# Kernel optimization log

Measured on AMD Instinct MI355X. Metric: run time of the kernel, lower is better.

The kernel has to match this reference:

```python
import jax, jax.numpy as jnp
import numpy as np

E = 8        # num experts
K = 2        # top-k
H = 1024     # hidden size
F = 3584     # intermediate (ffn) size
B, S = 1, 2048


def setup_inputs() -> dict:
    key = jax.random.key(0)
    ks = jax.random.split(key, 5)
    scale_h = 1.0 / np.sqrt(H)
    scale_f = 1.0 / np.sqrt(F)
    return {
        "hidden_states": jax.random.normal(ks[0], (B, S, H), jnp.float32),
        "gate_w": jax.random.normal(ks[1], (E, H), jnp.float32) * scale_h,  # Linear [out,in]
        "w1": jax.random.normal(ks[2], (E, F, H), jnp.float32) * scale_h,
        "w3": jax.random.normal(ks[3], (E, F, H), jnp.float32) * scale_h,
        "w2": jax.random.normal(ks[4], (E, H, F), jnp.float32) * scale_f,
    }


def reference(hidden_states, gate_w, w1, w3, w2):
    b, s, h = hidden_states.shape
    x = hidden_states.reshape(-1, h)                       # [T,H]
    T = x.shape[0]
    # Router: softmax over experts, top-k, renormalize
    router_logits = x @ gate_w.T                           # [T,E]
    routing_weights = jax.nn.softmax(router_logits.astype(jnp.float32), axis=-1)
    topk_w, topk_idx = jax.lax.top_k(routing_weights, K)   # [T,K]
    topk_w = topk_w / jnp.sum(topk_w, axis=-1, keepdims=True)
    # Per-token, per-expert combine weight (0 for unselected experts) --
    # matches the original mask-and-sum over all experts.
    tok = jnp.arange(T)
    expert_weights = jnp.zeros((T, E), jnp.float32).at[tok[:, None], topk_idx].add(topk_w)  # [T,E]
    # Dense per-expert SiLU-gated MLP over all tokens (as the reference loop does),
    # vectorized across experts.
    g = jnp.einsum("th,efh->etf", x, w1)                   # [E,T,F]
    u = jnp.einsum("th,efh->etf", x, w3)                   # [E,T,F]
    act = jax.nn.silu(g) * u                               # [E,T,F]
    y = jnp.einsum("etf,ehf->eth", act, w2)                # [E,T,H]
    out = jnp.einsum("eth,te->th", y, expert_weights.astype(y.dtype))  # [T,H]
    return out.reshape(b, s, h)
```

## Files before the change

kernel.cpp:

```cpp
#include <hip/hip_runtime.h>
#include <hip/hip_bf16.h>

#define T_TOK 2048
#define HID   1024
#define FF    3584
#define NE    8
#define TOPK  2
#define GRIDY 24

typedef __bf16 bf16x8 __attribute__((ext_vector_type(8)));
typedef float  f32x4  __attribute__((ext_vector_type(4)));
typedef unsigned short u16x8 __attribute__((ext_vector_type(8)));

#define WS_COUNTS   0u
#define WS_OFFSETS  64u
#define WS_TILECNT  128u
#define WS_TLE      256u
#define WS_TLM      512u
#define WS_TOPKI    4096u
#define WS_TOPKW    20480u
#define WS_SLOTPOS  36864u
#define WS_SLOTROW  53248u
#define WS_ROUTETOK 69632u
#define WS_XG       131072u
#define WS_ACT      (WS_XG + 4096u*1024u*2u)
#define WS_Y        (WS_ACT + 4096u*3584u*2u)
#define Y_STRIDE    (4096u*1024u)

static __device__ __forceinline__ unsigned short f2bf(float f) {
    unsigned int u = __builtin_bit_cast(unsigned int, f);
    u += 0x7FFFu + ((u >> 16) & 1u);
    return (unsigned short)(u >> 16);
}
static __device__ __forceinline__ unsigned int cvtpk(float lo, float hi) {
    unsigned int r;
    asm("v_cvt_pk_bf16_f32 %0, %1, %2" : "=v"(r) : "v"(lo), "v"(hi));
    return r;
}

__global__ __launch_bounds__(256) void k_router(
    const float* __restrict__ x, const float* __restrict__ gw,
    int* __restrict__ counts, int* __restrict__ topki,
    float* __restrict__ topkw, int* __restrict__ slotpos)
{
    int t = blockIdx.x * 4 + (threadIdx.x >> 6);
    int l = threadIdx.x & 63;
    const float* xr = x + (size_t)t * HID;
    float acc[NE];
#pragma unroll
    for (int e = 0; e < NE; ++e) acc[e] = 0.f;
#pragma unroll
    for (int i = 0; i < 4; ++i) {
        int h = l * 4 + i * 256;
        float4 xv = *(const float4*)(xr + h);
#pragma unroll
        for (int e = 0; e < NE; ++e) {
            float4 g = *(const float4*)(gw + e * HID + h);
            acc[e] += xv.x * g.x + xv.y * g.y + xv.z * g.z + xv.w * g.w;
        }
    }
#pragma unroll
    for (int e = 0; e < NE; ++e) {
#pragma unroll
        for (int off = 32; off; off >>= 1) acc[e] += __shfl_xor(acc[e], off);
    }
    if (l == 0) {
        float best = -1e30f, second = -1e30f;
        int bi = 0, si = 0;
#pragma unroll
        for (int e = 0; e < NE; ++e) {
            float v = acc[e];
            if (v > best) { second = best; si = bi; best = v; bi = e; }
            else if (v > second) { second = v; si = e; }
        }
        float w0 = 1.f / (1.f + __expf(second - best));
        float w1 = 1.f - w0;
        topki[2 * t] = bi;  topki[2 * t + 1] = si;
        topkw[2 * t] = w0;  topkw[2 * t + 1] = w1;
        slotpos[2 * t]     = atomicAdd(&counts[bi], 1);
        slotpos[2 * t + 1] = atomicAdd(&counts[si], 1);
    }
}

__global__ void k_prefix(const int* __restrict__ counts, int* __restrict__ offsets,
                         int* __restrict__ tle, int* __restrict__ tlm,
                         int* __restrict__ tilecnt) {
    if (threadIdx.x == 0) {
        int o = 0;
#pragma unroll
        for (int e = 0; e < NE; ++e) { offsets[e] = o; o += counts[e]; }
        int n = 0;
        for (int e = 0; e < NE; ++e) {
            int t = (counts[e] + 255) >> 8;
            for (int i = 0; i < t; ++i) { tle[n] = e; tlm[n] = i; ++n; }
        }
        tilecnt[0] = n;
    }
}

__global__ __launch_bounds__(256) void k_fillgather(
    const float* __restrict__ x, const int* __restrict__ topki,
    const int* __restrict__ slotpos, const int* __restrict__ offsets,
    int* __restrict__ routetok, int* __restrict__ slotrow,
    unsigned short* __restrict__ xg)
{
    int j = blockIdx.x;
    int e = topki[j];
    int row = offsets[e] + slotpos[j];
    int tok = j >> 1;
    if (threadIdx.x == 0) {
        routetok[row] = tok;
        slotrow[j] = row;
    }
    int c = threadIdx.x * 4;
    float4 v = *(const float4*)(x + (size_t)tok * HID + c);
    ushort4 o;
    o.x = f2bf(v.x); o.y = f2bf(v.y); o.z = f2bf(v.z); o.w = f2bf(v.w);
    int sc = c ^ ((row & 7) << 3);
    *(ushort4*)(xg + (size_t)row * HID + sc) = o;
}

__global__ __launch_bounds__(512, 4) void k_gemm1(
    const unsigned short* __restrict__ xg, const float* __restrict__ w1,
    const float* __restrict__ w3, const int* __restrict__ counts,
    const int* __restrict__ offsets, const int* __restrict__ tle,
    const int* __restrict__ tlm, const int* __restrict__ tilecnt,
    unsigned short* __restrict__ act)
{
    int d = blockIdx.x;
    int xcd = d & 7, s = d >> 3;
    int fhi = s % 7, by = s / 7;
    int fx = xcd + 8 * fhi;
    if (by >= tilecnt[0]) return;
    int e = tle[by];
    int rbase = tlm[by] * 256;
    int cnt = counts[e], obase = offsets[e];
    int fbase = fx * 64;

    __shared__ __align__(16) unsigned short lA[256 * 64];
    __shared__ __align__(16) unsigned short lB1[64 * 64];
    __shared__ __align__(16) unsigned short lB3[64 * 64];

    int tid = threadIdx.x;
    const int ra0 = tid >> 3, ca = (tid & 7) * 8;
    const int rb0 = tid >> 4, cb = (tid & 15) * 4;
    const unsigned short* pa[4];
#pragma unroll
    for (int i = 0; i < 4; ++i) {
        int r = obase + rbase + ra0 + 64 * i;
        if (r > 4095) r = 4095;
        pa[i] = xg + (size_t)r * HID + ca;
    }
    const float* w1e = w1 + ((size_t)e * FF + fbase) * HID;
    const float* w3e = w3 + ((size_t)e * FF + fbase) * HID;
    const float* pb1[2];
    const float* pb3[2];
    int wba[2];
#pragma unroll
    for (int i = 0; i < 2; ++i) {
        int row = rb0 + 32 * i;
        pb1[i] = w1e + (size_t)row * HID + cb;
        pb3[i] = w3e + (size_t)row * HID + cb;
        wba[i] = row * 64 + (cb ^ ((row & 7) << 3));
    }

    int lane = tid & 63, wv = tid >> 6, wr = wv >> 1, wc = wv & 1;
    int klane = (lane >> 4) * 8;
    int swzA = (((obase & 7) + (lane & 7)) & 7) << 3;
    int swzB = (lane & 7) << 3;
    f32x4 accg[4][2], accu[4][2];
#pragma unroll
    for (int m = 0; m < 4; ++m)
#pragma unroll
        for (int n = 0; n < 2; ++n) {
            accg[m][n] = (f32x4){0.f, 0.f, 0.f, 0.f};
            accu[m][n] = (f32x4){0.f, 0.f, 0.f, 0.f};
        }

    u16x8 ra[4]; float4 r1[2], r3[2];
#pragma unroll
    for (int i = 0; i < 4; ++i) ra[i] = *(const u16x8*)(pa[i]);
#pragma unroll
    for (int i = 0; i < 2; ++i) { r1[i] = *(const float4*)(pb1[i]); r3[i] = *(const float4*)(pb3[i]); }

    for (int kt = 0; kt < HID / 64; ++kt) {
#pragma unroll
        for (int i = 0; i < 4; ++i)
            *(u16x8*)(lA + (ra0 + 64 * i) * 64 + ca) = ra[i];
#pragma unroll
        for (int i = 0; i < 2; ++i) {
            uint2 p;
            p.x = cvtpk(r1[i].x, r1[i].y); p.y = cvtpk(r1[i].z, r1[i].w);
            *(uint2*)(lB1 + wba[i]) = p;
            p.x = cvtpk(r3[i].x, r3[i].y); p.y = cvtpk(r3[i].z, r3[i].w);
            *(uint2*)(lB3 + wba[i]) = p;
        }
        __syncthreads();
        if (kt < HID / 64 - 1) {
            int kof = (kt + 1) * 64;
#pragma unroll
            for (int i = 0; i < 4; ++i) ra[i] = *(const u16x8*)(pa[i] + kof);
#pragma unroll
            for (int i = 0; i < 2; ++i) {
                r1[i] = *(const float4*)(pb1[i] + kof);
                r3[i] = *(const float4*)(pb3[i] + kof);
            }
        }
#pragma unroll
        for (int kk = 0; kk < 64; kk += 32) {
            int kc = kk + klane;
            int kA = kc ^ swzA, kB = kc ^ swzB;
            bf16x8 a[4], b1[2], b3[2];
#pragma unroll
            for (int m = 0; m < 4; ++m)
                a[m] = *(const bf16x8*)(lA + (wr * 64 + m * 16 + (lane & 15)) * 64 + kA);
#pragma unroll
            for (int n = 0; n < 2; ++n) {
                b1[n] = *(const bf16x8*)(lB1 + (wc * 32 + n * 16 + (lane & 15)) * 64 + kB);
                b3[n] = *(const bf16x8*)(lB3 + (wc * 32 + n * 16 + (lane & 15)) * 64 + kB);
            }
#pragma unroll
            for (int m = 0; m < 4; ++m)
#pragma unroll
                for (int n = 0; n < 2; ++n) {
                    accg[m][n] = __builtin_amdgcn_mfma_f32_16x16x32_bf16(a[m], b1[n], accg[m][n], 0, 0, 0);
                    accu[m][n] = __builtin_amdgcn_mfma_f32_16x16x32_bf16(a[m], b3[n], accu[m][n], 0, 0, 0);
                }
        }
        __syncthreads();
    }

#pragma unroll
    for (int m = 0; m < 4; ++m)
#pragma unroll
        for (int n = 0; n < 2; ++n)
#pragma unroll
            for (int r = 0; r < 4; ++r) {
                int lr = wr * 64 + m * 16 + (lane >> 4) * 4 + r;
                if (rbase + lr < cnt) {
                    float g = accg[m][n][r], u = accu[m][n][r];
                    float s = g / (1.f + __expf(-g));
                    int row = obase + rbase + lr;
                    int col = fbase + wc * 32 + n * 16 + (lane & 15);
                    int scol = col ^ ((row & 7) << 3);
                    act[(size_t)row * FF + scol] = f2bf(s * u);
                }
            }
}

__global__ __launch_bounds__(512, 4) void k_gemm2(
    const unsigned short* __restrict__ act, const float* __restrict__ w2,
    const int* __restrict__ counts, const int* __restrict__ offsets,
    const int* __restrict__ tle, const int* __restrict__ tlm,
    const int* __restrict__ tilecnt, float* __restrict__ y, int ks)
{
    int d = blockIdx.x;
    int hx = d & 7, s = d >> 3;
    int z = s % 3, by = s / 3;
    if (by >= tilecnt[0]) return;
    if (z >= ks) return;
    int e = tle[by];
    int rbase = tlm[by] * 256;
    int cnt = counts[e], obase = offsets[e];
    int hbase = hx * 128;
    const int KTOT = FF / 64;
    int per = (KTOT + ks - 1) / ks;
    int kt0 = z * per;
    int ktn = (KTOT < kt0 + per ? KTOT : kt0 + per) - kt0;
    int kb0 = kt0 * 64;

    __shared__ __align__(16) unsigned short lA[256 * 64];
    __shared__ __align__(16) unsigned short lB[128 * 64];

    int tid = threadIdx.x;
    const int ra0 = tid >> 3, ca = (tid & 7) * 8;
    const unsigned short* pa[4];
#pragma unroll
    for (int i = 0; i < 4; ++i) {
        int r = obase + rbase + ra0 + 64 * i;
        if (r > 4095) r = 4095;
        pa[i] = act + (size_t)r * FF + kb0 + ca;
    }
    int hr = tid >> 2, cbf = (tid & 3) * 16;
    const float* pb = w2 + ((size_t)e * HID + hbase + hr) * FF + kb0 + cbf;
    int wbb[2];
#pragma unroll
    for (int g = 0; g < 2; ++g)
        wbb[g] = hr * 64 + ((cbf + g * 8) ^ ((hr & 7) << 3));

    int lane = tid & 63, wv = tid >> 6;
    int wr = wv & 3, wc = wv >> 2;
    int klane = (lane >> 4) * 8;
    int swzA = (((obase & 7) + (lane & 7)) & 7) << 3;
    int swzB = (lane & 7) << 3;
    f32x4 acc[4][4];
#pragma unroll
    for (int m = 0; m < 4; ++m)
#pragma unroll
        for (int n = 0; n < 4; ++n) acc[m][n] = (f32x4){0.f, 0.f, 0.f, 0.f};

    u16x8 ra[4]; float4 rw[4];
#pragma unroll
    for (int i = 0; i < 4; ++i) ra[i] = *(const u16x8*)(pa[i]);
#pragma unroll
    for (int j = 0; j < 4; ++j) rw[j] = *(const float4*)(pb + 4 * j);

    for (int kt = 0; kt < ktn; ++kt) {
#pragma unroll
        for (int i = 0; i < 4; ++i)
            *(u16x8*)(lA + (ra0 + 64 * i) * 64 + ca) = ra[i];
#pragma unroll
        for (int g = 0; g < 2; ++g) {
            uint4 q;
            q.x = cvtpk(rw[2 * g].x, rw[2 * g].y);
            q.y = cvtpk(rw[2 * g].z, rw[2 * g].w);
            q.z = cvtpk(rw[2 * g + 1].x, rw[2 * g + 1].y);
            q.w = cvtpk(rw[2 * g + 1].z, rw[2 * g + 1].w);
            *(uint4*)(lB + wbb[g]) = q;
        }
        __syncthreads();
        if (kt < ktn - 1) {
            int kof = (kt + 1) * 64;
#pragma unroll
            for (int i = 0; i < 4; ++i) ra[i] = *(const u16x8*)(pa[i] + kof);
#pragma unroll
            for (int j = 0; j < 4; ++j) rw[j] = *(const float4*)(pb + kof + 4 * j);
        }
#pragma unroll
        for (int kk = 0; kk < 64; kk += 32) {
            int kc = kk + klane;
            int kA = kc ^ swzA, kB = kc ^ swzB;
            bf16x8 a[4], b[4];
#pragma unroll
            for (int m = 0; m < 4; ++m)
                a[m] = *(const bf16x8*)(lA + (wr * 64 + m * 16 + (lane & 15)) * 64 + kA);
#pragma unroll
            for (int n = 0; n < 4; ++n)
                b[n] = *(const bf16x8*)(lB + (wc * 64 + n * 16 + (lane & 15)) * 64 + kB);
#pragma unroll
            for (int m = 0; m < 4; ++m)
#pragma unroll
                for (int n = 0; n < 4; ++n)
                    acc[m][n] = __builtin_amdgcn_mfma_f32_16x16x32_bf16(a[m], b[n], acc[m][n], 0, 0, 0);
        }
        __syncthreads();
    }

    float* yz = y + (size_t)z * Y_STRIDE;
#pragma unroll
    for (int m = 0; m < 4; ++m)
#pragma unroll
        for (int n = 0; n < 4; ++n)
#pragma unroll
            for (int r = 0; r < 4; ++r) {
                int lr = wr * 64 + m * 16 + (lane >> 4) * 4 + r;
                if (rbase + lr < cnt) {
                    int col = hbase + wc * 64 + n * 16 + (lane & 15);
                    yz[(size_t)(obase + rbase + lr) * HID + col] = acc[m][n][r];
                }
            }
}

__global__ void k_combine(const float* __restrict__ y, const int* __restrict__ slotrow,
                          const float* __restrict__ topkw, float* __restrict__ out, int ks) {
    int j = blockIdx.x * blockDim.x + threadIdx.x;
    int t = j >> 8, c = j & 255;
    int r0 = slotrow[2 * t], r1 = slotrow[2 * t + 1];
    float w0 = topkw[2 * t], w1 = topkw[2 * t + 1];
    float4 a = {0.f, 0.f, 0.f, 0.f}, b = {0.f, 0.f, 0.f, 0.f};
    for (int z = 0; z < ks; ++z) {
        const float4* yz = (const float4*)(y + (size_t)z * Y_STRIDE);
        float4 av = yz[(size_t)r0 * 256 + c];
        float4 bv = yz[(size_t)r1 * 256 + c];
        a.x += av.x; a.y += av.y; a.z += av.z; a.w += av.w;
        b.x += bv.x; b.y += bv.y; b.z += bv.z; b.w += bv.w;
    }
    float4 o;
    o.x = w0 * a.x + w1 * b.x;
    o.y = w0 * a.y + w1 * b.y;
    o.z = w0 * a.z + w1 * b.z;
    o.w = w0 * a.w + w1 * b.w;
    ((float4*)out)[j] = o;
}

extern "C" void kernel_launch(void* const* d_in, const int* in_sizes, int n_in,
                              void* d_out, int out_size, void* d_ws, size_t ws_size,
                              hipStream_t stream) {
    const float* x  = (const float*)d_in[0];
    const float* gw = (const float*)d_in[1];
    const float* w1 = (const float*)d_in[2];
    const float* w3 = (const float*)d_in[3];
    const float* w2 = (const float*)d_in[4];
    float* out = (float*)d_out;

    char* ws = (char*)d_ws;
    int*   counts   = (int*)(ws + WS_COUNTS);
    int*   offsets  = (int*)(ws + WS_OFFSETS);
    int*   tilecnt  = (int*)(ws + WS_TILECNT);
    int*   tle      = (int*)(ws + WS_TLE);
    int*   tlm      = (int*)(ws + WS_TLM);
    int*   topki    = (int*)(ws + WS_TOPKI);
    float* topkw    = (float*)(ws + WS_TOPKW);
    int*   slotpos  = (int*)(ws + WS_SLOTPOS);
    int*   slotrow  = (int*)(ws + WS_SLOTROW);
    int*   routetok = (int*)(ws + WS_ROUTETOK);
    unsigned short* xg   = (unsigned short*)(ws + WS_XG);
    unsigned short* actb = (unsigned short*)(ws + WS_ACT);
    float* yb = (float*)(ws + WS_Y);

    size_t ybytes = (size_t)Y_STRIDE * 4;
    int ks = (ws_size >= (size_t)WS_Y + 3 * ybytes) ? 3 : 2;

    hipMemsetAsync(counts, 0, 64, stream);
    k_router<<<T_TOK / 4, 256, 0, stream>>>(x, gw, counts, topki, topkw, slotpos);
    k_prefix<<<1, 64, 0, stream>>>(counts, offsets, tle, tlm, tilecnt);
    k_fillgather<<<T_TOK * TOPK, 256, 0, stream>>>(x, topki, slotpos, offsets, routetok, slotrow, xg);
    k_gemm1<<<56 * GRIDY, 512, 0, stream>>>(xg, w1, w3, counts, offsets, tle, tlm, tilecnt, actb);
    k_gemm2<<<8 * 3 * GRIDY, 512, 0, stream>>>(actb, w2, counts, offsets, tle, tlm, tilecnt, yb, ks);
    k_combine<<<2048, 256, 0, stream>>>(yb, slotrow, topkw, out, ks);
}
```

Before: 265.2 us.

## Process pairs of row tiles per gemm1 block and switch to 2D/3D grids

gemm1 blocks now loop over up to two consecutive 256-row tiles of the same expert, reusing one block's weight column slice, with a new paired tile list built in the prefix kernel. Both GEMMs drop the XCD-interleaved 1D block index mapping in favour of plain multi-dimensional grids. The aim is fewer gemm1 blocks and a partial reuse of weight addressing per block. The trade-off is less parallelism and a serialized second tile in each block, with no weight data kept across tiles (it is reloaded from global). Dropping the XCD-aware ordering may also hurt L2 locality.

Result: slower. 306.0 us (+15.4%).

```diff
diff --git a/kernel.cpp b/kernel.cpp
--- a/kernel.cpp
+++ b/kernel.cpp
@@ -6,7 +6,8 @@
 #define FF    3584
 #define NE    8
 #define TOPK  2
-#define GRIDY 24
+#define GRIDY  24
+#define GRIDYP 16
 
 typedef __bf16 bf16x8 __attribute__((ext_vector_type(8)));
 typedef float  f32x4  __attribute__((ext_vector_type(4)));
@@ -17,6 +18,8 @@
 #define WS_TILECNT  128u
 #define WS_TLE      256u
 #define WS_TLM      512u
+#define WS_TLPE     1280u
+#define WS_TLPM     1536u
 #define WS_TOPKI    4096u
 #define WS_TOPKW    20480u
 #define WS_SLOTPOS  36864u
@@ -84,17 +87,19 @@
 
 __global__ void k_prefix(const int* __restrict__ counts, int* __restrict__ offsets,
                          int* __restrict__ tle, int* __restrict__ tlm,
+                         int* __restrict__ tlpe, int* __restrict__ tlpm,
                          int* __restrict__ tilecnt) {
     if (threadIdx.x == 0) {
         int o = 0;
 #pragma unroll
         for (int e = 0; e < NE; ++e) { offsets[e] = o; o += counts[e]; }
-        int n = 0;
+        int n = 0, np = 0;
         for (int e = 0; e < NE; ++e) {
             int t = (counts[e] + 255) >> 8;
             for (int i = 0; i < t; ++i) { tle[n] = e; tlm[n] = i; ++n; }
-        }
-        tilecnt[0] = n;
+            for (int i = 0; i < t; i += 2) { tlpe[np] = e; tlpm[np] = i; ++np; }
+        }
+        tilecnt[0] = n; tilecnt[1] = np;
     }
 }
 
@@ -123,19 +128,17 @@
 __global__ __launch_bounds__(512, 4) void k_gemm1(
     const unsigned short* __restrict__ xg, const float* __restrict__ w1,
     const float* __restrict__ w3, const int* __restrict__ counts,
-    const int* __restrict__ offsets, const int* __restrict__ tle,
-    const int* __restrict__ tlm, const int* __restrict__ tilecnt,
+    const int* __restrict__ offsets, const int* __restrict__ tlpe,
+    const int* __restrict__ tlpm, const int* __restrict__ tilecnt,
     unsigned short* __restrict__ act)
 {
-    int d = blockIdx.x;
-    int xcd = d & 7, s = d >> 3;
-    int fhi = s % 7, by = s / 7;
-    int fx = xcd + 8 * fhi;
-    if (by >= tilecnt[0]) return;
-    int e = tle[by];
-    int rbase = tlm[by] * 256;
+    int bp = blockIdx.y;
+    if (bp >= tilecnt[1]) return;
+    int e = tlpe[bp];
+    int m0 = tlpm[bp];
     int cnt = counts[e], obase = offsets[e];
-    int fbase = fx * 64;
+    int ntile = (cnt + 255) >> 8;
+    int fbase = blockIdx.x * 64;
 
     __shared__ __align__(16) unsigned short lA[256 * 64];
     __shared__ __align__(16) unsigned short lB1[64 * 64];
@@ -144,13 +147,6 @@
     int tid = threadIdx.x;
     const int ra0 = tid >> 3, ca = (tid & 7) * 8;
     const int rb0 = tid >> 4, cb = (tid & 15) * 4;
-    const unsigned short* pa[4];
-#pragma unroll
-    for (int i = 0; i < 4; ++i) {
-        int r = obase + rbase + ra0 + 64 * i;
-        if (r > 4095) r = 4095;
-        pa[i] = xg + (size_t)r * HID + ca;
-    }
     const float* w1e = w1 + ((size_t)e * FF + fbase) * HID;
     const float* w3e = w3 + ((size_t)e * FF + fbase) * HID;
     const float* pb1[2];
@@ -168,84 +164,99 @@
     int klane = (lane >> 4) * 8;
     int swzA = (((obase & 7) + (lane & 7)) & 7) << 3;
     int swzB = (lane & 7) << 3;
-    f32x4 accg[4][2], accu[4][2];
-#pragma unroll
-    for (int m = 0; m < 4; ++m)
-#pragma unroll
-        for (int n = 0; n < 2; ++n) {
-            accg[m][n] = (f32x4){0.f, 0.f, 0.f, 0.f};
-            accu[m][n] = (f32x4){0.f, 0.f, 0.f, 0.f};
-        }
-
-    u16x8 ra[4]; float4 r1[2], r3[2];
-#pragma unroll
-    for (int i = 0; i < 4; ++i) ra[i] = *(const u16x8*)(pa[i]);
-#pragma unroll
-    for (int i = 0; i < 2; ++i) { r1[i] = *(const float4*)(pb1[i]); r3[i] = *(const float4*)(pb3[i]); }
-
-    for (int kt = 0; kt < HID / 64; ++kt) {
-#pragma unroll
-        for (int i = 0; i < 4; ++i)
-            *(u16x8*)(lA + (ra0 + 64 * i) * 64 + ca) = ra[i];
-#pragma unroll
-        for (int i = 0; i < 2; ++i) {
-            uint2 p;
-            p.x = cvtpk(r1[i].x, r1[i].y); p.y = cvtpk(r1[i].z, r1[i].w);
-            *(uint2*)(lB1 + wba[i]) = p;
-            p.x = cvtpk(r3[i].x, r3[i].y); p.y = cvtpk(r3[i].z, r3[i].w);
-            *(uint2*)(lB3 + wba[i]) = p;
-        }
-        __syncthreads();
-        if (kt < HID / 64 - 1) {
-            int kof = (kt + 1) * 64;
-#pragma unroll
-            for (int i = 0; i < 4; ++i) ra[i] = *(const u16x8*)(pa[i] + kof);
+
+    for (int h = 0; h < 2; ++h) {
+        int mt = m0 + h;
+        if (mt >= ntile) break;
+        int rbase = mt * 256;
+
+        const unsigned short* pa[4];
+#pragma unroll
+        for (int i = 0; i < 4; ++i) {
+            int r = obase + rbase + ra0 + 64 * i;
+            if (r > 4095) r = 4095;
+            pa[i] = xg + (size_t)r * HID + ca;
+        }
+
+        f32x4 accg[4][2], accu[4][2];
+#pragma unroll
+        for (int m = 0; m < 4; ++m)
+#pragma unroll
+            for (int n = 0; n < 2; ++n) {
+                accg[m][n] = (f32x4){0.f, 0.f, 0.f, 0.f};
+                accu[m][n] = (f32x4){0.f, 0.f, 0.f, 0.f};
+            }
+
+        u16x8 ra[4]; float4 r1[2], r3[2];
+#pragma unroll
+        for (int i = 0; i < 4; ++i) ra[i] = *(const u16x8*)(pa[i]);
+#pragma unroll
+        for (int i = 0; i < 2; ++i) { r1[i] = *(const float4*)(pb1[i]); r3[i] = *(const float4*)(pb3[i]); }
+
+        for (int kt = 0; kt < HID / 64; ++kt) {
+#pragma unroll
+            for (int i = 0; i < 4; ++i)
+                *(u16x8*)(lA + (ra0 + 64 * i) * 64 + ca) = ra[i];
 #pragma unroll
             for (int i = 0; i < 2; ++i) {
-                r1[i] = *(const float4*)(pb1[i] + kof);
-                r3[i] = *(const float4*)(pb3[i] + kof);
+                uint2 p;
+                p.x = cvtpk(r1[i].x, r1[i].y); p.y = cvtpk(r1[i].z, r1[i].w);
+                *(uint2*)(lB1 + wba[i]) = p;
+                p.x = cvtpk(r3[i].x, r3[i].y); p.y = cvtpk(r3[i].z, r3[i].w);
+                *(uint2*)(lB3 + wba[i]) = p;
             }
-        }
-#pragma unroll
-        for (int kk = 0; kk < 64; kk += 32) {
-            int kc = kk + klane;
-            int kA = kc ^ swzA, kB = kc ^ swzB;
-            bf16x8 a[4], b1[2], b3[2];
-#pragma unroll
-            for (int m = 0; m < 4; ++m)
-                a[m] = *(const bf16x8*)(lA + (wr * 64 + m * 16 + (lane & 15)) * 64 + kA);
-#pragma unroll
-            for (int n = 0; n < 2; ++n) {
-                b1[n] = *(const bf16x8*)(lB1 + (wc * 32 + n * 16 + (lane & 15)) * 64 + kB);
-                b3[n] = *(const bf16x8*)(lB3 + (wc * 32 + n * 16 + (lane & 15)) * 64 + kB);
-            }
-#pragma unroll
-            for (int m = 0; m < 4; ++m)
-#pragma unroll
-                for (int n = 0; n < 2; ++n) {
-                    accg[m][n] = __builtin_amdgcn_mfma_f32_16x16x32_bf16(a[m], b1[n], accg[m][n], 0, 0, 0);
-                    accu[m][n] = __builtin_amdgcn_mfma_f32_16x16x32_bf16(a[m], b3[n], accu[m][n], 0, 0, 0);
-                }
-        }
-        __syncthreads();
-    }
-
-#pragma unroll
-    for (int m = 0; m < 4; ++m)
-#pragma unroll
-        for (int n = 0; n < 2; ++n)
-#pragma unroll
-            for (int r = 0; r < 4; ++r) {
-                int lr = wr * 64 + m * 16 + (lane >> 4) * 4 + r;
-                if (rbase + lr < cnt) {
-                    float g = accg[m][n][r], u = accu[m][n][r];
-                    float s = g / (1.f + __expf(-g));
-                    int row = obase + rbase + lr;
-                    int col = fbase + wc * 32 + n * 16 + (lane & 15);
-                    int scol = col ^ ((row & 7) << 3);
-                    act[(size_t)row * FF + scol] = f2bf(s * u);
+            __syncthreads();
+            if (kt < HID / 64 - 1) {
+                int kof = (kt + 1) * 64;
+#pragma unroll
+                for (int i = 0; i < 4; ++i) ra[i] = *(const u16x8*)(pa[i] + kof);
+#pragma unroll
+                for (int i = 0; i < 2; ++i) {
+                    r1[i] = *(const float4*)(pb1[i] + kof);
+                    r3[i] = *(const float4*)(pb3[i] + kof);
                 }
             }
+#pragma unroll
+            for (int kk = 0; kk < 64; kk += 32) {
+                int kc = kk + klane;
+                int kA = kc ^ swzA, kB = kc ^ swzB;
+                bf16x8 a[4], b1[2], b3[2];
+#pragma unroll
+                for (int m = 0; m < 4; ++m)
+                    a[m] = *(const bf16x8*)(lA + (wr * 64 + m * 16 + (lane & 15)) * 64 + kA);
+#pragma unroll
+                for (int n = 0; n < 2; ++n) {
+                    b1[n] = *(const bf16x8*)(lB1 + (wc * 32 + n * 16 + (lane & 15)) * 64 + kB);
+                    b3[n] = *(const bf16x8*)(lB3 + (wc * 32 + n * 16 + (lane & 15)) * 64 + kB);
+                }
+#pragma unroll
+                for (int m = 0; m < 4; ++m)
+#pragma unroll
+                    for (int n = 0; n < 2; ++n) {
+                        accg[m][n] = __builtin_amdgcn_mfma_f32_16x16x32_bf16(a[m], b1[n], accg[m][n], 0, 0, 0);
+                        accu[m][n] = __builtin_amdgcn_mfma_f32_16x16x32_bf16(a[m], b3[n], accu[m][n], 0, 0, 0);
+                    }
+            }
+            __syncthreads();
+        }
+
+#pragma unroll
+        for (int m = 0; m < 4; ++m)
+#pragma unroll
+            for (int n = 0; n < 2; ++n)
+#pragma unroll
+                for (int r = 0; r < 4; ++r) {
+                    int lr = wr * 64 + m * 16 + (lane >> 4) * 4 + r;
+                    if (rbase + lr < cnt) {
+                        float g = accg[m][n][r], u = accu[m][n][r];
+                        float s = g / (1.f + __expf(-g));
+                        int row = obase + rbase + lr;
+                        int col = fbase + wc * 32 + n * 16 + (lane & 15);
+                        int scol = col ^ ((row & 7) << 3);
+                        act[(size_t)row * FF + scol] = f2bf(s * u);
+                    }
+                }
+    }
 }
 
 __global__ __launch_bounds__(512, 4) void k_gemm2(
@@ -254,15 +265,13 @@
     const int* __restrict__ tle, const int* __restrict__ tlm,
     const int* __restrict__ tilecnt, float* __restrict__ y, int ks)
 {
-    int d = blockIdx.x;
-    int hx = d & 7, s = d >> 3;
-    int z = s % 3, by = s / 3;
+    int by = blockIdx.y;
     if (by >= tilecnt[0]) return;
-    if (z >= ks) return;
     int e = tle[by];
     int rbase = tlm[by] * 256;
     int cnt = counts[e], obase = offsets[e];
-    int hbase = hx * 128;
+    int hbase = blockIdx.x * 128;
+    int z = blockIdx.z;
     const int KTOT = FF / 64;
     int per = (KTOT + ks - 1) / ks;
     int kt0 = z * per;
@@ -399,6 +408,8 @@
     int*   tilecnt  = (int*)(ws + WS_TILECNT);
     int*   tle      = (int*)(ws + WS_TLE);
     int*   tlm      = (int*)(ws + WS_TLM);
+    int*   tlpe     = (int*)(ws + WS_TLPE);
+    int*   tlpm     = (int*)(ws + WS_TLPM);
     int*   topki    = (int*)(ws + WS_TOPKI);
     float* topkw    = (float*)(ws + WS_TOPKW);
     int*   slotpos  = (int*)(ws + WS_SLOTPOS);
@@ -413,9 +424,9 @@
 
     hipMemsetAsync(counts, 0, 64, stream);
     k_router<<<T_TOK / 4, 256, 0, stream>>>(x, gw, counts, topki, topkw, slotpos);
-    k_prefix<<<1, 64, 0, stream>>>(counts, offsets, tle, tlm, tilecnt);
+    k_prefix<<<1, 64, 0, stream>>>(counts, offsets, tle, tlm, tlpe, tlpm, tilecnt);
     k_fillgather<<<T_TOK * TOPK, 256, 0, stream>>>(x, topki, slotpos, offsets, routetok, slotrow, xg);
-    k_gemm1<<<56 * GRIDY, 512, 0, stream>>>(xg, w1, w3, counts, offsets, tle, tlm, tilecnt, actb);
-    k_gemm2<<<8 * 3 * GRIDY, 512, 0, stream>>>(actb, w2, counts, offsets, tle, tlm, tilecnt, yb, ks);
+    k_gemm1<<<dim3(FF / 64, GRIDYP, 1), 512, 0, stream>>>(xg, w1, w3, counts, offsets, tlpe, tlpm, tilecnt, actb);
+    k_gemm2<<<dim3(HID / 128, GRIDY, ks), 512, 0, stream>>>(actb, w2, counts, offsets, tle, tlm, tilecnt, yb, ks);
     k_combine<<<2048, 256, 0, stream>>>(yb, slotrow, topkw, out, ks);
 }
```

## Widen gemm1 N-tile to 128 columns and drop XCD-aware block mapping

Applied to the files above, without the earlier changes.

The gate/up GEMM block tile grows from 256x64 to 256x128 along F, with the warp layout changed to 4x2 and each thread loading 32 contiguous fp32 weights. The goal is to halve how often the gathered activation tile is re-read from memory and to raise MFMA work per LDS sync. The cost is doubled accumulator registers (launch bounds drop from 4 to 2 blocks per SM) and fewer blocks. Both GEMMs also switch from a hand-linearised XCD-aware block index to a plain 2D/3D grid, which removes the explicit per-XCD L2 grouping.

Result: slower. 337.4 us (+27.2%).

```diff
diff --git a/kernel.cpp b/kernel.cpp
--- a/kernel.cpp
+++ b/kernel.cpp
@@ -120,30 +120,26 @@
     *(ushort4*)(xg + (size_t)row * HID + sc) = o;
 }
 
-__global__ __launch_bounds__(512, 4) void k_gemm1(
+__global__ __launch_bounds__(512, 2) void k_gemm1(
     const unsigned short* __restrict__ xg, const float* __restrict__ w1,
     const float* __restrict__ w3, const int* __restrict__ counts,
     const int* __restrict__ offsets, const int* __restrict__ tle,
     const int* __restrict__ tlm, const int* __restrict__ tilecnt,
     unsigned short* __restrict__ act)
 {
-    int d = blockIdx.x;
-    int xcd = d & 7, s = d >> 3;
-    int fhi = s % 7, by = s / 7;
-    int fx = xcd + 8 * fhi;
+    int by = blockIdx.y;
     if (by >= tilecnt[0]) return;
     int e = tle[by];
     int rbase = tlm[by] * 256;
     int cnt = counts[e], obase = offsets[e];
-    int fbase = fx * 64;
+    int fbase = blockIdx.x * 128;
 
     __shared__ __align__(16) unsigned short lA[256 * 64];
-    __shared__ __align__(16) unsigned short lB1[64 * 64];
-    __shared__ __align__(16) unsigned short lB3[64 * 64];
+    __shared__ __align__(16) unsigned short lB1[128 * 64];
+    __shared__ __align__(16) unsigned short lB3[128 * 64];
 
     int tid = threadIdx.x;
     const int ra0 = tid >> 3, ca = (tid & 7) * 8;
-    const int rb0 = tid >> 4, cb = (tid & 15) * 4;
     const unsigned short* pa[4];
 #pragma unroll
     for (int i = 0; i < 4; ++i) {
@@ -151,49 +147,46 @@
         if (r > 4095) r = 4095;
         pa[i] = xg + (size_t)r * HID + ca;
     }
-    const float* w1e = w1 + ((size_t)e * FF + fbase) * HID;
-    const float* w3e = w3 + ((size_t)e * FF + fbase) * HID;
-    const float* pb1[2];
-    const float* pb3[2];
-    int wba[2];
-#pragma unroll
-    for (int i = 0; i < 2; ++i) {
-        int row = rb0 + 32 * i;
-        pb1[i] = w1e + (size_t)row * HID + cb;
-        pb3[i] = w3e + (size_t)row * HID + cb;
-        wba[i] = row * 64 + (cb ^ ((row & 7) << 3));
-    }
-
-    int lane = tid & 63, wv = tid >> 6, wr = wv >> 1, wc = wv & 1;
+    int mb = tid >> 8, rb = (tid >> 1) & 127, kh = tid & 1;
+    const float* pb = (mb ? w3 : w1) + ((size_t)e * FF + fbase + rb) * HID + kh * 32;
+    unsigned short* lB = mb ? lB3 : lB1;
+    int wbb[4];
+#pragma unroll
+    for (int g = 0; g < 4; ++g)
+        wbb[g] = rb * 64 + ((kh * 32 + g * 8) ^ ((rb & 7) << 3));
+
+    int lane = tid & 63, wv = tid >> 6;
+    int wr = wv & 3, wc = wv >> 2;
     int klane = (lane >> 4) * 8;
     int swzA = (((obase & 7) + (lane & 7)) & 7) << 3;
     int swzB = (lane & 7) << 3;
-    f32x4 accg[4][2], accu[4][2];
+    f32x4 accg[4][4], accu[4][4];
 #pragma unroll
     for (int m = 0; m < 4; ++m)
 #pragma unroll
-        for (int n = 0; n < 2; ++n) {
+        for (int n = 0; n < 4; ++n) {
             accg[m][n] = (f32x4){0.f, 0.f, 0.f, 0.f};
             accu[m][n] = (f32x4){0.f, 0.f, 0.f, 0.f};
         }
 
-    u16x8 ra[4]; float4 r1[2], r3[2];
+    u16x8 ra[4]; float4 rw[8];
 #pragma unroll
     for (int i = 0; i < 4; ++i) ra[i] = *(const u16x8*)(pa[i]);
 #pragma unroll
-    for (int i = 0; i < 2; ++i) { r1[i] = *(const float4*)(pb1[i]); r3[i] = *(const float4*)(pb3[i]); }
+    for (int j = 0; j < 8; ++j) rw[j] = *(const float4*)(pb + 4 * j);
 
     for (int kt = 0; kt < HID / 64; ++kt) {
 #pragma unroll
         for (int i = 0; i < 4; ++i)
             *(u16x8*)(lA + (ra0 + 64 * i) * 64 + ca) = ra[i];
 #pragma unroll
-        for (int i = 0; i < 2; ++i) {
-            uint2 p;
-            p.x = cvtpk(r1[i].x, r1[i].y); p.y = cvtpk(r1[i].z, r1[i].w);
-            *(uint2*)(lB1 + wba[i]) = p;
-            p.x = cvtpk(r3[i].x, r3[i].y); p.y = cvtpk(r3[i].z, r3[i].w);
-            *(uint2*)(lB3 + wba[i]) = p;
+        for (int g = 0; g < 4; ++g) {
+            uint4 q;
+            q.x = cvtpk(rw[2 * g].x, rw[2 * g].y);
+            q.y = cvtpk(rw[2 * g].z, rw[2 * g].w);
+            q.z = cvtpk(rw[2 * g + 1].x, rw[2 * g + 1].y);
+            q.w = cvtpk(rw[2 * g + 1].z, rw[2 * g + 1].w);
+            *(uint4*)(lB + wbb[g]) = q;
         }
         __syncthreads();
         if (kt < HID / 64 - 1) {
@@ -201,30 +194,27 @@
 #pragma unroll
             for (int i = 0; i < 4; ++i) ra[i] = *(const u16x8*)(pa[i] + kof);
 #pragma unroll
-            for (int i = 0; i < 2; ++i) {
-                r1[i] = *(const float4*)(pb1[i] + kof);
-                r3[i] = *(const float4*)(pb3[i] + kof);
-            }
+            for (int j = 0; j < 8; ++j) rw[j] = *(const float4*)(pb + kof + 4 * j);
         }
 #pragma unroll
         for (int kk = 0; kk < 64; kk += 32) {
             int kc = kk + klane;
             int kA = kc ^ swzA, kB = kc ^ swzB;
-            bf16x8 a[4], b1[2], b3[2];
+            bf16x8 a[4], b1f[4], b3f[4];
 #pragma unroll
             for (int m = 0; m < 4; ++m)
                 a[m] = *(const bf16x8*)(lA + (wr * 64 + m * 16 + (lane & 15)) * 64 + kA);
 #pragma unroll
-            for (int n = 0; n < 2; ++n) {
-                b1[n] = *(const bf16x8*)(lB1 + (wc * 32 + n * 16 + (lane & 15)) * 64 + kB);
-                b3[n] = *(const bf16x8*)(lB3 + (wc * 32 + n * 16 + (lane & 15)) * 64 + kB);
+            for (int n = 0; n < 4; ++n) {
+                b1f[n] = *(const bf16x8*)(lB1 + (wc * 64 + n * 16 + (lane & 15)) * 64 + kB);
+                b3f[n] = *(const bf16x8*)(lB3 + (wc * 64 + n * 16 + (lane & 15)) * 64 + kB);
             }
 #pragma unroll
             for (int m = 0; m < 4; ++m)
 #pragma unroll
-                for (int n = 0; n < 2; ++n) {
-                    accg[m][n] = __builtin_amdgcn_mfma_f32_16x16x32_bf16(a[m], b1[n], accg[m][n], 0, 0, 0);
-                    accu[m][n] = __builtin_amdgcn_mfma_f32_16x16x32_bf16(a[m], b3[n], accu[m][n], 0, 0, 0);
+                for (int n = 0; n < 4; ++n) {
+                    accg[m][n] = __builtin_amdgcn_mfma_f32_16x16x32_bf16(a[m], b1f[n], accg[m][n], 0, 0, 0);
+                    accu[m][n] = __builtin_amdgcn_mfma_f32_16x16x32_bf16(a[m], b3f[n], accu[m][n], 0, 0, 0);
                 }
         }
         __syncthreads();
@@ -233,7 +223,7 @@
 #pragma unroll
     for (int m = 0; m < 4; ++m)
 #pragma unroll
-        for (int n = 0; n < 2; ++n)
+        for (int n = 0; n < 4; ++n)
 #pragma unroll
             for (int r = 0; r < 4; ++r) {
                 int lr = wr * 64 + m * 16 + (lane >> 4) * 4 + r;
@@ -241,7 +231,7 @@
                     float g = accg[m][n][r], u = accu[m][n][r];
                     float s = g / (1.f + __expf(-g));
                     int row = obase + rbase + lr;
-                    int col = fbase + wc * 32 + n * 16 + (lane & 15);
+                    int col = fbase + wc * 64 + n * 16 + (lane & 15);
                     int scol = col ^ ((row & 7) << 3);
                     act[(size_t)row * FF + scol] = f2bf(s * u);
                 }
@@ -254,15 +244,13 @@
     const int* __restrict__ tle, const int* __restrict__ tlm,
     const int* __restrict__ tilecnt, float* __restrict__ y, int ks)
 {
-    int d = blockIdx.x;
-    int hx = d & 7, s = d >> 3;
-    int z = s % 3, by = s / 3;
+    int by = blockIdx.y;
     if (by >= tilecnt[0]) return;
-    if (z >= ks) return;
     int e = tle[by];
     int rbase = tlm[by] * 256;
     int cnt = counts[e], obase = offsets[e];
-    int hbase = hx * 128;
+    int hbase = blockIdx.x * 128;
+    int z = blockIdx.z;
     const int KTOT = FF / 64;
     int per = (KTOT + ks - 1) / ks;
     int kt0 = z * per;
@@ -415,7 +403,7 @@
     k_router<<<T_TOK / 4, 256, 0, stream>>>(x, gw, counts, topki, topkw, slotpos);
     k_prefix<<<1, 64, 0, stream>>>(counts, offsets, tle, tlm, tilecnt);
     k_fillgather<<<T_TOK * TOPK, 256, 0, stream>>>(x, topki, slotpos, offsets, routetok, slotrow, xg);
-    k_gemm1<<<56 * GRIDY, 512, 0, stream>>>(xg, w1, w3, counts, offsets, tle, tlm, tilecnt, actb);
-    k_gemm2<<<8 * 3 * GRIDY, 512, 0, stream>>>(actb, w2, counts, offsets, tle, tlm, tilecnt, yb, ks);
+    k_gemm1<<<dim3(FF / 128, GRIDY, 1), 512, 0, stream>>>(xg, w1, w3, counts, offsets, tle, tlm, tilecnt, actb);
+    k_gemm2<<<dim3(HID / 128, GRIDY, ks), 512, 0, stream>>>(actb, w2, counts, offsets, tle, tlm, tilecnt, yb, ks);
     k_combine<<<2048, 256, 0, stream>>>(yb, slotrow, topkw, out, ks);
 }
```
